# Performance work log

Measured on AMD Instinct MI355X. Metric: run time of the kernel, lower is better.

## Reference

```python
import jax, jax.numpy as jnp
import numpy as np

B, S, D, H = 32, 512, 640, 10
DK = D // H           # 64
NUM_ITER = 3          # capsule routing iterations


def _proj(x, W, b):
    # [B,S,D] @ [D,D]^T -> split heads -> [B,H,S,DK]
    b_, s_, _ = x.shape
    return (x @ W.T + b).reshape(b_, s_, H, DK).transpose(0, 2, 1, 3)


def _squash(t, eps=1e-9):
    sn = jnp.sum(t * t, axis=-1, keepdims=True)
    return (sn / (1.0 + sn)) * t / jnp.sqrt(sn + eps)


def setup_inputs() -> dict:
    key0 = jax.random.key(0)
    ks = jax.random.split(key0, 12)
    s = 1.0 / np.sqrt(D)
    return {
        "query": jax.random.normal(ks[0], (B, S, D), jnp.float32),
        "key": jax.random.normal(ks[1], (B, S, D), jnp.float32),
        "value": jax.random.normal(ks[2], (B, S, D), jnp.float32),
        "mask": jax.random.randint(ks[3], (B, 1, S, S), 0, 2, jnp.int32),
        "adj": jax.random.uniform(ks[4], (B, S, S), jnp.float32),
        "layer": 2,
        "Wq": jax.random.normal(ks[5], (D, D), jnp.float32) * s,
        "bq": jnp.zeros((D,), jnp.float32),
        "Wk": jax.random.normal(ks[6], (D, D), jnp.float32) * s,
        "bk": jnp.zeros((D,), jnp.float32),
        "Wv": jax.random.normal(ks[7], (D, D), jnp.float32) * s,
        "bv": jnp.zeros((D,), jnp.float32),
        # capsule route weights: [num_capsules=1, num_route_nodes=H, DK, D]
        "route_weights": jax.random.normal(ks[8], (1, H, DK, D), jnp.float32) * 0.05,
    }


def reference(query, key, value, mask, adj, layer,
              Wq, bq, Wk, bk, Wv, bv, route_weights):
    q = _proj(query, Wq, bq)   # [B,H,S,DK]
    k = _proj(key, Wk, bk)
    v = _proj(value, Wv, bv)

    # scaled dot-product scores, adjacency + layer-dependent modulation
    scores = jnp.einsum('bhqd,bhkd->bhqk', q, k) / jnp.sqrt(jnp.float32(DK))
    scores = scores + adj[:, None, :, :] / jnp.float32(layer + 1)
    scores = jnp.where(mask == 0, jnp.float32(-1e9), scores)
    p_attn = jax.nn.softmax(scores, axis=-1)            # [B,H,S,S]
    x = jnp.einsum('bhqk,bhkd->bhqd', p_attn, v)        # [B,H,S,DK]

    # [B,H,S,DK] -> [B*S, H, DK]: per-token capsule routing over heads
    x = x.transpose(0, 2, 1, 3).reshape(B * S, H, DK)

    # priors: [num_caps=1, N, H(route nodes), D]
    priors = jnp.einsum('nri,crio->cnro', x, route_weights)
    logits = jnp.zeros(priors.shape[:-1] + (1,), priors.dtype)  # [1,N,H,1]
    out = None
    for i in range(NUM_ITER):
        probs = jax.nn.softmax(logits, axis=2)                  # over route nodes
        out = _squash(jnp.sum(probs * priors, axis=2, keepdims=True))  # [1,N,1,D]
        if i != NUM_ITER - 1:
            logits = logits + jnp.sum(priors * out, axis=-1, keepdims=True)

    return out.reshape(B, S, D)
```

## Files before the change

### kernel.cpp

```cpp
#include <hip/hip_runtime.h>
#include <stdint.h>

#define BB 32
#define SS 512
#define DD 640
#define HH 10
#define DKK 64
#define NTOK (BB*SS)

using f32x4  = __attribute__((ext_vector_type(4))) float;
using bf16x8 = __attribute__((ext_vector_type(8))) __bf16;
using u32x4  = __attribute__((ext_vector_type(4))) unsigned int;
using u32x2  = __attribute__((ext_vector_type(2))) unsigned int;
using u16x4  = __attribute__((ext_vector_type(4))) unsigned short;
using i32x4  = __attribute__((ext_vector_type(4))) int;

__device__ inline unsigned short f2bf(float f){
  union { float f; unsigned int u; } v; v.f=f;
  unsigned int u=v.u;
  u += 0x7FFFu + ((u>>16)&1u);
  return (unsigned short)(u>>16);
}
__device__ inline float bf2f(unsigned short s){
  union { unsigned int u; float f; } v; v.u = ((unsigned int)s)<<16;
  return v.f;
}
__device__ inline unsigned int cvtpk_bf16(float lo, float hi){
  unsigned int r;
  asm volatile("v_cvt_pk_bf16_f32 %0, %1, %2" : "=v"(r) : "v"(lo), "v"(hi));
  return r;
}
__device__ inline void gload_lds16(const unsigned short* g, unsigned short* l){
  __builtin_amdgcn_global_load_lds(
      (const __attribute__((address_space(1))) unsigned int*)g,
      (__attribute__((address_space(3))) unsigned int*)l, 16, 0, 0);
}

__global__ void convert_qkv(const float* __restrict__ q, const float* __restrict__ k,
                            const float* __restrict__ v,
                            unsigned short* __restrict__ xq, unsigned short* __restrict__ xk,
                            unsigned short* __restrict__ xv){
  int i = blockIdx.x*blockDim.x + threadIdx.x;
  const int n4 = (NTOK*DD)/4;
  for (; i < n4; i += gridDim.x*blockDim.x){
    f32x4 a = ((const f32x4*)q)[i];
    f32x4 b = ((const f32x4*)k)[i];
    f32x4 c = ((const f32x4*)v)[i];
    u16x4 ra, rb, rc;
    #pragma unroll
    for (int j=0;j<4;j++){ ra[j]=f2bf(a[j]); rb[j]=f2bf(b[j]); rc[j]=f2bf(c[j]); }
    ((u16x4*)xq)[i]=ra; ((u16x4*)xk)[i]=rb; ((u16x4*)xv)[i]=rc;
  }
}

__global__ void convert_w(const float* __restrict__ wq, const float* __restrict__ wk,
                          const float* __restrict__ wv, const float* __restrict__ rw,
                          unsigned short* __restrict__ bwq, unsigned short* __restrict__ bwk,
                          unsigned short* __restrict__ bwv, unsigned short* __restrict__ brwt,
                          unsigned short* __restrict__ brwtf){
  int i = blockIdx.x*blockDim.x + threadIdx.x;
  if (i < DD*DD){
    bwq[i]=f2bf(wq[i]); bwk[i]=f2bf(wk[i]); bwv[i]=f2bf(wv[i]);
    unsigned short rv = f2bf(rw[i]);
    const int kk = i / DD;
    const int o  = i % DD;
    brwt[o*DD + kk] = rv;
    const int r  = kk >> 6, ii = kk & 63;
    const int ks = ii >> 5, rem = ii & 31, g = rem >> 3, j = rem & 7;
    const int oT = o >> 4, l15o = o & 15;
    brwtf[(size_t)((oT*10 + r)*2 + ks)*512 + (g*16 + l15o)*8 + j] = rv;
  }
}

__global__ void bias_kernel(const int* __restrict__ mask, const float* __restrict__ adj,
                            const int* __restrict__ layer, unsigned short* __restrict__ biasT){
  float sc = 1.0f/(float)(layer[0]+1);
  int i = blockIdx.x*blockDim.x + threadIdx.x;
  const int n4 = (BB*SS*SS)/4;
  for (; i < n4; i += gridDim.x*blockDim.x){
    i32x4 m = ((const i32x4*)mask)[i];
    f32x4 a = ((const f32x4*)adj)[i];
    u16x4 r;
    #pragma unroll
    for (int j=0;j<4;j++) r[j] = m[j] ? f2bf(a[j]*sc) : f2bf(-1e9f);
    const int e  = i*4;
    const int bb = e >> 18;
    const int qq = (e >> 9) & 511;
    const int kk = e & 511;
    const int idx = (((bb*32 + (qq>>4))*32 + (kk>>4))<<8) + ((qq&15)<<4) + (kk&15);
    *(u16x4*)(biasT + idx) = r;
  }
}

#define BM 128
#define BN 128
#define BK 32

template<typename EPI>
__device__ inline void gemm_body(const unsigned short* __restrict__ A,
                                 const unsigned short* __restrict__ W,
                                 int m0, int n0, EPI&& epi)
{
  __shared__ unsigned short As[2][BM*BK];
  __shared__ unsigned short Ws[2][BN*BK];
  const int tid  = threadIdx.x;
  const int lane = tid & 63;
  const int wave = tid >> 6;
  const int wr   = (wave >> 1) * 64;
  const int wc   = (wave & 1) * 64;
  const int l15  = lane & 15;
  const int g    = lane >> 4;

  f32x4 acc[4][4];
  #pragma unroll
  for (int i=0;i<4;i++)
    #pragma unroll
    for (int j=0;j<4;j++){ f32x4 z = {0.f,0.f,0.f,0.f}; acc[i][j]=z; }

  const int srow  = (lane >> 2);
  const int sunit = (lane & 3) ^ ((lane >> 3) & 3);
  const unsigned short* Ag0 = A + (int64_t)(m0 + wave*32 + srow)*DD + sunit*8;
  const unsigned short* Ag1 = A + (int64_t)(m0 + wave*32 + 16 + srow)*DD + sunit*8;
  const unsigned short* Wg0 = W + (int64_t)(n0 + wave*32 + srow)*DD + sunit*8;
  const unsigned short* Wg1 = W + (int64_t)(n0 + wave*32 + 16 + srow)*DD + sunit*8;

  auto stage = [&](int buf, int k0){
    gload_lds16(Ag0 + k0, As[buf] + wave*1024);
    gload_lds16(Ag1 + k0, As[buf] + wave*1024 + 512);
    gload_lds16(Wg0 + k0, Ws[buf] + wave*1024);
    gload_lds16(Wg1 + k0, Ws[buf] + wave*1024 + 512);
  };

  const int fro = (g ^ ((l15 >> 1) & 3)) * 8;

  stage(0, 0);
  int it = 0;
  for (int k0 = 0; k0 < DD; k0 += BK, it++){
    const int buf = it & 1;
    __syncthreads();
    if (k0 + BK < DD) stage(buf^1, k0 + BK);
    bf16x8 af[4], wf[4];
    #pragma unroll
    for (int m=0;m<4;m++) af[m] = *(const bf16x8*)&As[buf][(wr + m*16 + l15)*BK + fro];
    #pragma unroll
    for (int n=0;n<4;n++) wf[n] = *(const bf16x8*)&Ws[buf][(wc + n*16 + l15)*BK + fro];
    #pragma unroll
    for (int m=0;m<4;m++)
      #pragma unroll
      for (int n=0;n<4;n++)
        acc[m][n] = __builtin_amdgcn_mfma_f32_16x16x32_bf16(af[m], wf[n], acc[m][n], 0,0,0);
  }

  #pragma unroll
  for (int m=0;m<4;m++){
    const int rowbase = m0 + wr + m*16 + g*4;
    #pragma unroll
    for (int n=0;n<4;n++){
      const int col = n0 + wc + n*16 + l15;
      #pragma unroll
      for (int r=0;r<4;r++)
        epi(rowbase + r, col, acc[m][n][r]);
    }
  }
}

__global__ __launch_bounds__(256)
void qkv_gemm(const unsigned short* __restrict__ Xq, const unsigned short* __restrict__ Xk,
              const unsigned short* __restrict__ Xv,
              const unsigned short* __restrict__ bWq, const unsigned short* __restrict__ bWk,
              const unsigned short* __restrict__ bWv,
              const float* __restrict__ bq, const float* __restrict__ bk,
              const float* __restrict__ bv,
              unsigned short* __restrict__ qbuf, unsigned short* __restrict__ kbuf,
              unsigned short* __restrict__ vTbuf)
{
  const int y   = blockIdx.y;
  const int sel = y / 5;
  const int n0  = (y % 5) * BN;
  const int m0  = blockIdx.x * BM;
  const unsigned short* A = sel==0 ? Xq  : sel==1 ? Xk  : Xv;
  const unsigned short* W = sel==0 ? bWq : sel==1 ? bWk : bWv;
  const float*          bb= sel==0 ? bq  : sel==1 ? bk  : bv;
  unsigned short* outp    = sel==0 ? qbuf : kbuf;

  gemm_body(A, W, m0, n0, [&](int row, int col, float v){
    float val = v + bb[col];
    int b=row>>9, s=row&511, h=col>>6, dk=col&63;
    if (sel < 2)
      outp[(((int64_t)(b*HH + h))*SS + s)*DKK + dk] = f2bf(val);
    else
      vTbuf[(((int64_t)(b*HH + h))*DKK + dk)*SS + s] = f2bf(val);
  });
}

__global__ __launch_bounds__(256)
void final_gemm(const unsigned short* __restrict__ A, const unsigned short* __restrict__ W,
                float* __restrict__ outp)
{
  gemm_body(A, W, blockIdx.x*BM, blockIdx.y*BN, [&](int row, int col, float v){
    outp[(int64_t)row*DD + col] = v;
  });
}

__global__ __launch_bounds__(256)
void attn_kernel(const unsigned short* __restrict__ qb, const unsigned short* __restrict__ kb,
                 const unsigned short* __restrict__ vT, const unsigned short* __restrict__ biasT,
                 unsigned short* __restrict__ xout)
{
  __shared__ unsigned short SH[20480];
  unsigned short* Kl = SH;
  unsigned short* Vl = SH + 8192;
  char* Pall = (char*)(SH + 16384);

  const int tid  = threadIdx.x;
  const int lane = tid & 63;
  const int wave = tid >> 6;
  const int l15  = lane & 15;
  const int g    = lane >> 4;

  const int orig = blockIdx.x;
  const int wgid = (orig & 7)*320 + (orig >> 3);
  const int h  = wgid % 10;
  const int qt = (wgid / 10) & 7;
  const int b  = wgid / 80;
  const int bh = b*HH + h;

  const unsigned short* Q  = qb + (int64_t)bh*SS*DKK;
  const unsigned short* K  = kb + (int64_t)bh*SS*DKK;
  const unsigned short* V  = vT + (int64_t)bh*DKK*SS;
  const unsigned short* Bt = biasT + (int64_t)((b*32 + qt*4 + wave)*32)*256
                           + l15*16 + g*4;

  const int q0 = qt*64 + wave*16;
  char* Pb = Pall + wave*2048;

  const int srow8 = lane >> 3;
  const int sunit = (lane & 7) ^ (srow8 & 7);

  bf16x8 qf[2];
  #pragma unroll
  for (int ks=0; ks<2; ks++)
    qf[ks] = *(const bf16x8*)(Q + (q0 + l15)*DKK + ks*32 + g*8);

  auto stage = [&](int c, int buf){
    #pragma unroll
    for (int c2=0;c2<2;c2++){
      const int i = wave*2 + c2;
      gload_lds16(K + (int64_t)(c*64 + i*8 + srow8)*DKK + sunit*8,
                  Kl + buf*4096 + i*512);
      gload_lds16(V + (int64_t)(i*8 + srow8)*SS + c*64 + sunit*8,
                  Vl + buf*4096 + i*512);
    }
  };

  float lsum = 0.f;
  f32x4 oacc[4];
  #pragma unroll
  for (int n=0;n<4;n++){ f32x4 z={0.f,0.f,0.f,0.f}; oacc[n]=z; }

  u16x4 bvc[4], bvn[4];
  #pragma unroll
  for (int j=0;j<4;j++) bvc[j] = *(const u16x4*)(Bt + j*256);

  stage(0, 0);
  for (int c = 0; c < 8; c++){
    const int buf = c & 1;
    __syncthreads();
    if (c < 7){
      stage(c+1, buf^1);
      #pragma unroll
      for (int j=0;j<4;j++) bvn[j] = *(const u16x4*)(Bt + ((c+1)*4 + j)*256);
    }

    f32x4 sc[4];
    #pragma unroll
    for (int j=0;j<4;j++){ f32x4 z={0.f,0.f,0.f,0.f}; sc[j]=z; }
    #pragma unroll
    for (int ks=0; ks<2; ks++){
      #pragma unroll
      for (int j=0;j<4;j++){
        bf16x8 kf = *(const bf16x8*)((char*)(Kl + buf*4096)
                     + (j*16 + l15)*128 + (((ks*4+g) ^ (l15&7))*16));
        sc[j] = __builtin_amdgcn_mfma_f32_16x16x32_bf16(kf, qf[ks], sc[j], 0,0,0);
      }
    }
    #pragma unroll
    for (int j=0;j<4;j++){
      float p[4];
      #pragma unroll
      for (int r=0;r<4;r++){
        float s = __builtin_fmaf(sc[j][r], 0.125f, bf2f(bvc[j][r]));
        p[r] = __expf(s - 8.0f);
        lsum += p[r];
      }
      unsigned int w0 = cvtpk_bf16(p[0], p[1]);
      unsigned int w1 = cvtpk_bf16(p[2], p[3]);
      const int kk = j*16 + g*4;
      const int sw = (kk >> 3) ^ (l15 & 7);
      u32x2 w; w[0]=w0; w[1]=w1;
      *(u32x2*)(Pb + l15*128 + sw*16 + (kk&7)*2) = w;
    }
    #pragma unroll
    for (int kt=0; kt<2; kt++){
      bf16x8 pf = *(const bf16x8*)(Pb + l15*128 + (((kt*4+g) ^ (l15&7))*16));
      #pragma unroll
      for (int n=0;n<4;n++){
        bf16x8 vf = *(const bf16x8*)((char*)(Vl + buf*4096)
                     + (n*16 + l15)*128 + (((kt*4+g) ^ (l15&7))*16));
        oacc[n] = __builtin_amdgcn_mfma_f32_16x16x32_bf16(pf, vf, oacc[n], 0,0,0);
      }
    }
    #pragma unroll
    for (int j=0;j<4;j++) bvc[j] = bvn[j];
  }

  lsum += __shfl_xor(lsum, 16);
  lsum += __shfl_xor(lsum, 32);
  const float inv = 1.0f / lsum;
  float invr[4];
  #pragma unroll
  for (int r=0;r<4;r++) invr[r] = __shfl(inv, g*4 + r);

  #pragma unroll
  for (int n=0;n<4;n++){
    const int dk = n*16 + l15;
    #pragma unroll
    for (int r=0;r<4;r++){
      const int qrow = q0 + g*4 + r;
      const int ntok = b*SS + qrow;
      xout[(int64_t)ntok*DD + h*DKK + dk] = f2bf(oacc[n][r] * invr[r]);
    }
  }
}

__global__ __launch_bounds__(256)
void gram_part(const unsigned short* __restrict__ x,
               const unsigned short* __restrict__ RWTf,
               float* __restrict__ Gpart)
{
  __shared__ unsigned short Xl[16*664];
  __shared__ float Gp[4][16][57];

  const int tid  = threadIdx.x;
  const int lane = tid & 63;
  const int wave = tid >> 6;
  const int l15  = lane & 15;
  const int g    = lane >> 4;
  const int tok0 = blockIdx.x * 16;
  const int oc   = blockIdx.y;

  #pragma unroll
  for (int rd=0; rd<5; rd++){
    const int idx = rd*2048 + tid*8;
    const int tk  = idx / 640;
    const int cl  = idx - tk*640;
    u32x4 vv = *(const u32x4*)(x + (int64_t)tok0*640 + idx);
    *(u32x4*)&Xl[tk*664 + cl] = vv;
  }
  __syncthreads();

  float Gacc[55];
  #pragma unroll
  for (int p=0;p<55;p++) Gacc[p]=0.f;

  #pragma unroll
  for (int ot2=0; ot2<2; ot2++){
    const int oTile = oc*8 + wave*2 + ot2;
    const unsigned short* base = RWTf + (size_t)oTile*10240;
    f32x4 P[10];
    #pragma unroll
    for (int r=0;r<10;r++){ f32x4 z={0.f,0.f,0.f,0.f}; P[r]=z; }
    #pragma unroll
    for (int r=0;r<10;r++){
      #pragma unroll
      for (int ks=0;ks<2;ks++){
        bf16x8 af = *(const bf16x8*)&base[(r*2+ks)*512 + lane*8];
        bf16x8 xf = *(const bf16x8*)&Xl[l15*664 + r*64 + ks*32 + g*8];
        P[r] = __builtin_amdgcn_mfma_f32_16x16x32_bf16(af, xf, P[r], 0,0,0);
      }
    }
    #pragma unroll
    for (int r=0;r<10;r++)
      #pragma unroll
      for (int rp=r; rp<10; rp++){
        const int T = r*10 - r*(r-1)/2 + (rp-r);
        Gacc[T] += P[r][0]*P[rp][0] + P[r][1]*P[rp][1]
                 + P[r][2]*P[rp][2] + P[r][3]*P[rp][3];
      }
  }
  #pragma unroll
  for (int p=0;p<55;p++){
    Gacc[p] += __shfl_xor(Gacc[p], 16);
    Gacc[p] += __shfl_xor(Gacc[p], 32);
  }
  if (lane < 16){
    #pragma unroll
    for (int p=0;p<55;p++) Gp[wave][lane][p] = Gacc[p];
  }
  __syncthreads();
  {
    const int gtok = tid & 15;
    for (int p = tid>>4; p < 55; p += 16)
      Gpart[((size_t)oc*NTOK + tok0 + gtok)*56 + p]
        = Gp[0][gtok][p]+Gp[1][gtok][p]+Gp[2][gtok][p]+Gp[3][gtok][p];
  }
}

__global__ __launch_bounds__(256)
void route_xw(const float* __restrict__ Gpart, const unsigned short* __restrict__ x,
              unsigned short* __restrict__ xw)
{
  __shared__ float Gfin[16][57];
  __shared__ float Pr[16][10];
  __shared__ float Dm[16][10];
  __shared__ float Lg[16][10];
  __shared__ float wl[16][10];

  const int tid  = threadIdx.x;
  const int tok0 = blockIdx.x * 16;

  {
    const int gtok = tid & 15;
    for (int p = tid>>4; p < 55; p += 16){
      float s = 0.f;
      #pragma unroll
      for (int oc=0; oc<5; oc++)
        s += Gpart[((size_t)oc*NTOK + tok0 + gtok)*56 + p];
      Gfin[gtok][p] = s;
    }
  }
  __syncthreads();

  const int tok = tid >> 4, rp = tid & 15;
  const bool act = rp < 10;
  float grow[10]; float Lr = 0.f;
  if (act){
    #pragma unroll
    for (int r=0;r<10;r++){
      const int lo = r < rp ? r : rp, hi = r < rp ? rp : r;
      grow[r] = Gfin[tok][lo*10 - lo*(lo-1)/2 + (hi-lo)];
    }
    Pr[tok][rp] = 0.1f;
  }
  __syncthreads();
  for (int it=0; it<3; it++){
    float d = 0.f;
    if (act){
      #pragma unroll
      for (int r=0;r<10;r++) d += grow[r]*Pr[tok][r];
      Dm[tok][rp] = d;
    }
    __syncthreads();
    if (act){
      float sn = 0.f;
      #pragma unroll
      for (int r=0;r<10;r++) sn += Dm[tok][r]*Pr[tok][r];
      const float sc = (sn/(1.f+sn))*rsqrtf(sn+1e-9f);
      if (it < 2){ Lr += sc*d; Lg[tok][rp] = Lr; }
      else        wl[tok][rp] = sc*Pr[tok][rp];
    }
    __syncthreads();
    if (it < 2){
      if (act){
        float mx = Lg[tok][0];
        #pragma unroll
        for (int r=1;r<10;r++) mx = fmaxf(mx, Lg[tok][r]);
        float se = 0.f;
        #pragma unroll
        for (int r=0;r<10;r++) se += __expf(Lg[tok][r]-mx);
        Pr[tok][rp] = __expf(Lr-mx)/se;
      }
      __syncthreads();
    }
  }

  #pragma unroll
  for (int e=0; e<5; e++){
    const int idx = e*2048 + tid*8;
    const int tk  = idx / 640;
    const int cl  = idx - tk*640;
    const float w = wl[tk][cl>>6];
    u16x4 a = *(const u16x4*)(x + (int64_t)tok0*640 + idx);
    u16x4 b = *(const u16x4*)(x + (int64_t)tok0*640 + idx + 4);
    u32x4 o;
    o[0] = cvtpk_bf16(bf2f(a[0])*w, bf2f(a[1])*w);
    o[1] = cvtpk_bf16(bf2f(a[2])*w, bf2f(a[3])*w);
    o[2] = cvtpk_bf16(bf2f(b[0])*w, bf2f(b[1])*w);
    o[3] = cvtpk_bf16(bf2f(b[2])*w, bf2f(b[3])*w);
    *(u32x4*)&xw[(int64_t)tok0*640 + idx] = o;
  }
}

extern "C" void kernel_launch(void* const* d_in, const int* in_sizes, int n_in,
                              void* d_out, int out_size, void* d_ws, size_t ws_size,
                              hipStream_t stream)
{
  (void)in_sizes; (void)n_in; (void)out_size; (void)ws_size;
  const float* q    = (const float*)d_in[0];
  const float* k    = (const float*)d_in[1];
  const float* v    = (const float*)d_in[2];
  const int*   mask = (const int*)d_in[3];
  const float* adj  = (const float*)d_in[4];
  const int*   layer= (const int*)d_in[5];
  const float* Wq   = (const float*)d_in[6];
  const float* bq   = (const float*)d_in[7];
  const float* Wk   = (const float*)d_in[8];
  const float* bk   = (const float*)d_in[9];
  const float* Wv   = (const float*)d_in[10];
  const float* bv   = (const float*)d_in[11];
  const float* rw   = (const float*)d_in[12];

  char* ws = (char*)d_ws;
  size_t off = 0;
  auto alloc = [&](size_t sz)->char*{ char* p = ws + off; off += (sz + 255) & ~(size_t)255; return p; };
  const size_t SZX = (size_t)NTOK*DD*2;
  unsigned short* Xq    = (unsigned short*)alloc(SZX);
  unsigned short* Xk    = (unsigned short*)alloc(SZX);
  unsigned short* Xv    = (unsigned short*)alloc(SZX);
  unsigned short* bWq   = (unsigned short*)alloc((size_t)DD*DD*2);
  unsigned short* bWk   = (unsigned short*)alloc((size_t)DD*DD*2);
  unsigned short* bWv   = (unsigned short*)alloc((size_t)DD*DD*2);
  unsigned short* bRWT  = (unsigned short*)alloc((size_t)DD*DD*2);
  unsigned short* bRWTf = (unsigned short*)alloc((size_t)DD*DD*2);
  unsigned short* qbuf  = (unsigned short*)alloc(SZX);
  unsigned short* kbuf  = (unsigned short*)alloc(SZX);
  unsigned short* vTbuf = (unsigned short*)alloc(SZX);
  unsigned short* biasb = (unsigned short*)alloc((size_t)BB*SS*SS*2);
  float*          Gpart = (float*)alloc((size_t)5*NTOK*56*4);
  unsigned short* xout  = Xq;
  unsigned short* xw    = Xk;

  convert_qkv<<<2048,256,0,stream>>>(q,k,v,Xq,Xk,Xv);
  convert_w<<<1600,256,0,stream>>>(Wq,Wk,Wv,rw,bWq,bWk,bWv,bRWT,bRWTf);
  bias_kernel<<<2048,256,0,stream>>>(mask,adj,layer,biasb);

  dim3 gq(NTOK/BM, 15);
  qkv_gemm<<<gq,256,0,stream>>>(Xq,Xk,Xv,bWq,bWk,bWv,bq,bk,bv,qbuf,kbuf,vTbuf);

  attn_kernel<<<2560,256,0,stream>>>(qbuf,kbuf,vTbuf,biasb,xout);

  dim3 gp(NTOK/16, 5);
  gram_part<<<gp,256,0,stream>>>(xout,bRWTf,Gpart);
  route_xw<<<NTOK/16,256,0,stream>>>(Gpart,xout,xw);

  dim3 gf(NTOK/BM, DD/BN);
  final_gemm<<<gf,256,0,stream>>>(xw,bRWT,(float*)d_out);
}
```

Measured before the change: 298.5 us.

## Merge prep kernels and vectorize GEMM epilogues via swapped MFMA operands

The three conversion and bias kernels are merged into one launch, with block index ranges choosing the task. The GEMM body gains a template flag that swaps the MFMA A/B operands, so each lane holds four consecutive output columns. The Q/K and final GEMM epilogues can then write packed bf16 pairs or float4 vectors instead of scalar stores. The V projection is split into its own kernel, which packs four consecutive sequence positions for the transposed store. This removes two launches and many narrow scattered stores, at the cost of an extra launch for V and more code paths.

```diff
diff --git a/kernel.cpp b/kernel.cpp
--- a/kernel.cpp
+++ b/kernel.cpp
@@ -30,65 +30,69 @@
   asm volatile("v_cvt_pk_bf16_f32 %0, %1, %2" : "=v"(r) : "v"(lo), "v"(hi));
   return r;
 }
-__device__ inline void gload_lds16(const unsigned short* g, unsigned short* l){
+__device__ inline void gload_lds16(const void* g, void* l){
   __builtin_amdgcn_global_load_lds(
       (const __attribute__((address_space(1))) unsigned int*)g,
       (__attribute__((address_space(3))) unsigned int*)l, 16, 0, 0);
 }
 
-__global__ void convert_qkv(const float* __restrict__ q, const float* __restrict__ k,
+__global__ void prep_kernel(const float* __restrict__ q, const float* __restrict__ k,
                             const float* __restrict__ v,
+                            const int* __restrict__ mask, const float* __restrict__ adj,
+                            const int* __restrict__ layer,
+                            const float* __restrict__ wq, const float* __restrict__ wk,
+                            const float* __restrict__ wv, const float* __restrict__ rw,
                             unsigned short* __restrict__ xq, unsigned short* __restrict__ xk,
-                            unsigned short* __restrict__ xv){
-  int i = blockIdx.x*blockDim.x + threadIdx.x;
-  const int n4 = (NTOK*DD)/4;
-  for (; i < n4; i += gridDim.x*blockDim.x){
-    f32x4 a = ((const f32x4*)q)[i];
-    f32x4 b = ((const f32x4*)k)[i];
-    f32x4 c = ((const f32x4*)v)[i];
-    u16x4 ra, rb, rc;
-    #pragma unroll
-    for (int j=0;j<4;j++){ ra[j]=f2bf(a[j]); rb[j]=f2bf(b[j]); rc[j]=f2bf(c[j]); }
-    ((u16x4*)xq)[i]=ra; ((u16x4*)xk)[i]=rb; ((u16x4*)xv)[i]=rc;
-  }
-}
-
-__global__ void convert_w(const float* __restrict__ wq, const float* __restrict__ wk,
-                          const float* __restrict__ wv, const float* __restrict__ rw,
-                          unsigned short* __restrict__ bwq, unsigned short* __restrict__ bwk,
-                          unsigned short* __restrict__ bwv, unsigned short* __restrict__ brwt,
-                          unsigned short* __restrict__ brwtf){
-  int i = blockIdx.x*blockDim.x + threadIdx.x;
-  if (i < DD*DD){
-    bwq[i]=f2bf(wq[i]); bwk[i]=f2bf(wk[i]); bwv[i]=f2bf(wv[i]);
-    unsigned short rv = f2bf(rw[i]);
-    const int kk = i / DD;
-    const int o  = i % DD;
-    brwt[o*DD + kk] = rv;
-    const int r  = kk >> 6, ii = kk & 63;
-    const int ks = ii >> 5, rem = ii & 31, g = rem >> 3, j = rem & 7;
-    const int oT = o >> 4, l15o = o & 15;
-    brwtf[(size_t)((oT*10 + r)*2 + ks)*512 + (g*16 + l15o)*8 + j] = rv;
-  }
-}
-
-__global__ void bias_kernel(const int* __restrict__ mask, const float* __restrict__ adj,
-                            const int* __restrict__ layer, unsigned short* __restrict__ biasT){
-  float sc = 1.0f/(float)(layer[0]+1);
-  int i = blockIdx.x*blockDim.x + threadIdx.x;
-  const int n4 = (BB*SS*SS)/4;
-  for (; i < n4; i += gridDim.x*blockDim.x){
-    i32x4 m = ((const i32x4*)mask)[i];
-    f32x4 a = ((const f32x4*)adj)[i];
-    u16x4 r;
-    #pragma unroll
-    for (int j=0;j<4;j++) r[j] = m[j] ? f2bf(a[j]*sc) : f2bf(-1e9f);
-    const int e  = i*4;
-    const int bb = e >> 18;
-    const int qq = (e >> 9) & 511;
-    const int kk = e & 511;
-    const int idx = (((bb*32 + (qq>>4))*32 + (kk>>4))<<8) + ((qq&15)<<4) + (kk&15);
-    *(u16x4*)(biasT + idx) = r;
+                            unsigned short* __restrict__ xv,
+                            unsigned short* __restrict__ bwq, unsigned short* __restrict__ bwk,
+                            unsigned short* __restrict__ bwv, unsigned short* __restrict__ brwt,
+                            unsigned short* __restrict__ brwtf,
+                            unsigned short* __restrict__ biasT)
+{
+  const int bid = blockIdx.x;
+  const int tid = threadIdx.x;
+  if (bid < 2048){
+    int i = bid*256 + tid;
+    const int n4 = (NTOK*DD)/4;
+    for (; i < n4; i += 2048*256){
+      f32x4 a = ((const f32x4*)q)[i];
+      f32x4 b = ((const f32x4*)k)[i];
+      f32x4 c = ((const f32x4*)v)[i];
+      u16x4 ra, rb, rc;
+      #pragma unroll
+      for (int j=0;j<4;j++){ ra[j]=f2bf(a[j]); rb[j]=f2bf(b[j]); rc[j]=f2bf(c[j]); }
+      ((u16x4*)xq)[i]=ra; ((u16x4*)xk)[i]=rb; ((u16x4*)xv)[i]=rc;
+    }
+  } else if (bid < 3648){
+    const int i = (bid-2048)*256 + tid;
+    if (i < DD*DD){
+      bwq[i]=f2bf(wq[i]); bwk[i]=f2bf(wk[i]); bwv[i]=f2bf(wv[i]);
+      unsigned short rv = f2bf(rw[i]);
+      const int kk = i / DD;
+      const int o  = i % DD;
+      brwt[o*DD + kk] = rv;
+      const int r  = kk >> 6, ii = kk & 63;
+      const int ks = ii >> 5, rem = ii & 31, g = rem >> 3, j = rem & 7;
+      const int oT = o >> 4, l15o = o & 15;
+      brwtf[(size_t)((oT*10 + r)*2 + ks)*512 + (g*16 + l15o)*8 + j] = rv;
+    }
+  } else {
+    float sc = 1.0f/(float)(layer[0]+1);
+    int i = (bid-3648)*256 + tid;
+    const int n4 = (BB*SS*SS)/4;
+    for (; i < n4; i += 2048*256){
+      i32x4 m = ((const i32x4*)mask)[i];
+      f32x4 a = ((const f32x4*)adj)[i];
+      u16x4 r;
+      #pragma unroll
+      for (int j=0;j<4;j++) r[j] = m[j] ? f2bf(a[j]*sc) : f2bf(-1e9f);
+      const int e  = i*4;
+      const int bb = e >> 18;
+      const int qq = (e >> 9) & 511;
+      const int kk = e & 511;
+      const int idx = (((bb*32 + (qq>>4))*32 + (kk>>4))<<8) + ((qq&15)<<4) + (kk&15);
+      *(u16x4*)(biasT + idx) = r;
+    }
   }
 }
 
@@ -96,7 +100,7 @@
 #define BN 128
 #define BK 32
 
-template<typename EPI>
+template<bool SWAP, typename EPI>
 __device__ inline void gemm_body(const unsigned short* __restrict__ A,
                                  const unsigned short* __restrict__ W,
                                  int m0, int n0, EPI&& epi)
@@ -147,49 +151,71 @@
     #pragma unroll
     for (int m=0;m<4;m++)
       #pragma unroll
-      for (int n=0;n<4;n++)
-        acc[m][n] = __builtin_amdgcn_mfma_f32_16x16x32_bf16(af[m], wf[n], acc[m][n], 0,0,0);
-  }
-
-  #pragma unroll
-  for (int m=0;m<4;m++){
-    const int rowbase = m0 + wr + m*16 + g*4;
-    #pragma unroll
-    for (int n=0;n<4;n++){
-      const int col = n0 + wc + n*16 + l15;
-      #pragma unroll
-      for (int r=0;r<4;r++)
-        epi(rowbase + r, col, acc[m][n][r]);
-    }
-  }
+      for (int n=0;n<4;n++){
+        if constexpr (SWAP)
+          acc[m][n] = __builtin_amdgcn_mfma_f32_16x16x32_bf16(wf[n], af[m], acc[m][n], 0,0,0);
+        else
+          acc[m][n] = __builtin_amdgcn_mfma_f32_16x16x32_bf16(af[m], wf[n], acc[m][n], 0,0,0);
+      }
+  }
+
+  #pragma unroll
+  for (int m=0;m<4;m++)
+    #pragma unroll
+    for (int n=0;n<4;n++)
+      epi(m, n, acc[m][n]);
 }
 
 __global__ __launch_bounds__(256)
-void qkv_gemm(const unsigned short* __restrict__ Xq, const unsigned short* __restrict__ Xk,
-              const unsigned short* __restrict__ Xv,
-              const unsigned short* __restrict__ bWq, const unsigned short* __restrict__ bWk,
-              const unsigned short* __restrict__ bWv,
-              const float* __restrict__ bq, const float* __restrict__ bk,
-              const float* __restrict__ bv,
-              unsigned short* __restrict__ qbuf, unsigned short* __restrict__ kbuf,
-              unsigned short* __restrict__ vTbuf)
+void qk_gemm(const unsigned short* __restrict__ Xq, const unsigned short* __restrict__ Xk,
+             const unsigned short* __restrict__ bWq, const unsigned short* __restrict__ bWk,
+             const float* __restrict__ bq, const float* __restrict__ bk,
+             unsigned short* __restrict__ qbuf, unsigned short* __restrict__ kbuf)
 {
   const int y   = blockIdx.y;
   const int sel = y / 5;
   const int n0  = (y % 5) * BN;
   const int m0  = blockIdx.x * BM;
-  const unsigned short* A = sel==0 ? Xq  : sel==1 ? Xk  : Xv;
-  const unsigned short* W = sel==0 ? bWq : sel==1 ? bWk : bWv;
-  const float*          bb= sel==0 ? bq  : sel==1 ? bk  : bv;
-  unsigned short* outp    = sel==0 ? qbuf : kbuf;
-
-  gemm_body(A, W, m0, n0, [&](int row, int col, float v){
-    float val = v + bb[col];
-    int b=row>>9, s=row&511, h=col>>6, dk=col&63;
-    if (sel < 2)
-      outp[(((int64_t)(b*HH + h))*SS + s)*DKK + dk] = f2bf(val);
-    else
-      vTbuf[(((int64_t)(b*HH + h))*DKK + dk)*SS + s] = f2bf(val);
+  const unsigned short* A = sel ? Xk  : Xq;
+  const unsigned short* W = sel ? bWk : bWq;
+  const float* bb         = sel ? bk  : bq;
+  unsigned short* outp    = sel ? kbuf : qbuf;
+
+  const int lane = threadIdx.x & 63, wave = threadIdx.x >> 6;
+  const int wr = (wave>>1)*64, wc = (wave&1)*64, l15 = lane&15, g = lane>>4;
+
+  gemm_body<true>(A, W, m0, n0, [&](int m, int n, const f32x4& a){
+    const int token = m0 + wr + m*16 + l15;
+    const int b = token >> 9, s = token & 511;
+    const int wcol0 = n0 + wc + n*16 + g*4;
+    const int h = wcol0 >> 6, dk0 = wcol0 & 63;
+    f32x4 bv4 = *(const f32x4*)(bb + wcol0);
+    u32x2 w;
+    w[0] = cvtpk_bf16(a[0]+bv4[0], a[1]+bv4[1]);
+    w[1] = cvtpk_bf16(a[2]+bv4[2], a[3]+bv4[3]);
+    *(u32x2*)&outp[(((int64_t)(b*HH + h))*SS + s)*DKK + dk0] = w;
+  });
+}
+
+__global__ __launch_bounds__(256)
+void v_gemm(const unsigned short* __restrict__ Xv, const unsigned short* __restrict__ bWv,
+            const float* __restrict__ bv, unsigned short* __restrict__ vTbuf)
+{
+  const int n0 = blockIdx.y * BN;
+  const int m0 = blockIdx.x * BM;
+  const int lane = threadIdx.x & 63, wave = threadIdx.x >> 6;
+  const int wr = (wave>>1)*64, wc = (wave&1)*64, l15 = lane&15, g = lane>>4;
+
+  gemm_body<false>(Xv, bWv, m0, n0, [&](int m, int n, const f32x4& a){
+    const int row0 = m0 + wr + m*16 + g*4;
+    const int b = row0 >> 9, s0 = row0 & 511;
+    const int col = n0 + wc + n*16 + l15;
+    const int h = col >> 6, dk = col & 63;
+    const float bvv = bv[col];
+    u32x2 w;
+    w[0] = cvtpk_bf16(a[0]+bvv, a[1]+bvv);
+    w[1] = cvtpk_bf16(a[2]+bvv, a[3]+bvv);
+    *(u32x2*)&vTbuf[(((int64_t)(b*HH + h))*DKK + dk)*SS + s0] = w;
   });
 }
 
@@ -197,8 +223,14 @@
 void final_gemm(const unsigned short* __restrict__ A, const unsigned short* __restrict__ W,
                 float* __restrict__ outp)
 {
-  gemm_body(A, W, blockIdx.x*BM, blockIdx.y*BN, [&](int row, int col, float v){
-    outp[(int64_t)row*DD + col] = v;
+  const int m0 = blockIdx.x * BM, n0 = blockIdx.y * BN;
+  const int lane = threadIdx.x & 63, wave = threadIdx.x >> 6;
+  const int wr = (wave>>1)*64, wc = (wave&1)*64, l15 = lane&15, g = lane>>4;
+
+  gemm_body<true>(A, W, m0, n0, [&](int m, int n, const f32x4& a){
+    const int token = m0 + wr + m*16 + l15;
+    const int o0 = n0 + wc + n*16 + g*4;
+    *(f32x4*)&outp[(int64_t)token*DD + o0] = a;
   });
 }
 
@@ -530,12 +562,13 @@
   unsigned short* xout  = Xq;
   unsigned short* xw    = Xk;
 
-  convert_qkv<<<2048,256,0,stream>>>(q,k,v,Xq,Xk,Xv);
-  convert_w<<<1600,256,0,stream>>>(Wq,Wk,Wv,rw,bWq,bWk,bWv,bRWT,bRWTf);
-  bias_kernel<<<2048,256,0,stream>>>(mask,adj,layer,biasb);
-
-  dim3 gq(NTOK/BM, 15);
-  qkv_gemm<<<gq,256,0,stream>>>(Xq,Xk,Xv,bWq,bWk,bWv,bq,bk,bv,qbuf,kbuf,vTbuf);
+  prep_kernel<<<5696,256,0,stream>>>(q,k,v,mask,adj,layer,Wq,Wk,Wv,rw,
+                                     Xq,Xk,Xv,bWq,bWk,bWv,bRWT,bRWTf,biasb);
+
+  dim3 gqk(NTOK/BM, 10);
+  qk_gemm<<<gqk,256,0,stream>>>(Xq,Xk,bWq,bWk,bq,bk,qbuf,kbuf);
+  dim3 gv(NTOK/BM, 5);
+  v_gemm<<<gv,256,0,stream>>>(Xv,bWv,bv,vTbuf);
 
   attn_kernel<<<2560,256,0,stream>>>(qbuf,kbuf,vTbuf,biasb,xout);
 
```

Result: faster. 289.1 us (-3.2%).
